# Kernel optimization log

Hardware: AMD Instinct MI355X
Metric: run time of the kernel (lower is better)

Reference implementation:

```python
import jax, jax.numpy as jnp
import numpy as np

N = 20000      # nodes
E = 640000     # edges (before self loops)
IN = 256       # in_channels == out_channels (forced by classifier size 4*in)
H1, C1 = 8, 16   # conv1: heads=8, out=16 -> concat 128
H2, C2 = 1, 256  # conv2: heads=1, out=out_channels
B = 4096       # article pairs
NEG_SLOPE = 0.2  # PyG GATv2Conv default negative_slope


def setup_inputs() -> dict:
    key = jax.random.key(0)
    ks = jax.random.split(key, 24)
    s = 0.05
    inp = {
        "gnn_x": jax.random.normal(ks[0], (N, IN), jnp.float32),
        "vanilla_x": jax.random.normal(ks[1], (N, IN), jnp.float32),
        "edge_src": jax.random.randint(ks[2], (E,), 0, N, jnp.int32),
        "edge_dst": jax.random.randint(ks[3], (E,), 0, N, jnp.int32),
        "a1_idx": jax.random.randint(ks[4], (B,), 0, N, jnp.int64),
        "a2_idx": jax.random.randint(ks[5], (B,), 0, N, jnp.int64),
        # conv1 params (lin_l, lin_r, att, bias)
        "Wl1": jax.random.normal(ks[6], (IN, H1 * C1), jnp.float32) * s,
        "bl1": jnp.zeros((H1 * C1,), jnp.float32),
        "Wr1": jax.random.normal(ks[7], (IN, H1 * C1), jnp.float32) * s,
        "br1": jnp.zeros((H1 * C1,), jnp.float32),
        "att1": jax.random.normal(ks[8], (H1, C1), jnp.float32) * s,
        "bias1": jnp.zeros((H1 * C1,), jnp.float32),
        # conv2 params
        "Wl2": jax.random.normal(ks[9], (H1 * C1, H2 * C2), jnp.float32) * s,
        "bl2": jnp.zeros((H2 * C2,), jnp.float32),
        "Wr2": jax.random.normal(ks[10], (H1 * C1, H2 * C2), jnp.float32) * s,
        "br2": jnp.zeros((H2 * C2,), jnp.float32),
        "att2": jax.random.normal(ks[11], (H2, C2), jnp.float32) * s,
        "bias2": jnp.zeros((H2 * C2,), jnp.float32),
        # classifier
        "Wc": jax.random.normal(ks[12], (4 * IN, 1), jnp.float32) * s,
        "bc": jnp.zeros((1,), jnp.float32),
    }
    return inp


def _gatv2_layer(x, src, dst, Wl, bl, Wr, br, att, bias):
    """GATv2Conv: x_l = lin_l(x)[src], x_r = lin_r(x)[dst];
    e = att . leaky_relu(x_l + x_r); segment softmax over dst; scatter-add x_l*alpha."""
    n = x.shape[0]
    h, c = att.shape
    xl = (x @ Wl + bl).reshape(n, h, c)
    xr = (x @ Wr + br).reshape(n, h, c)
    # per-edge attention logits [E, H]
    e = jnp.einsum('ehc,hc->eh', jax.nn.leaky_relu(xl[src] + xr[dst], NEG_SLOPE), att)
    # segment softmax over destination nodes (self loops guarantee non-empty segments)
    emax = jax.ops.segment_max(e, dst, num_segments=n)
    ex = jnp.exp(e - emax[dst])
    denom = jax.ops.segment_sum(ex, dst, num_segments=n)
    alpha = ex / denom[dst]                      # [E, H]
    out = jax.ops.segment_sum(alpha[:, :, None] * xl[src], dst, num_segments=n)  # [N,H,C]
    return out.reshape(n, h * c) + bias          # concat=True (heads=1 identical)


def reference(gnn_x, vanilla_x, Wl1, bl1, Wr1, br1, att1, bias1,
              Wl2, bl2, Wr2, br2, att2, bias2, Wc, bc,
              edge_src, edge_dst, a1_idx, a2_idx):
    n = gnn_x.shape[0]
    loops = jnp.arange(n, dtype=edge_src.dtype)
    src = jnp.concatenate([edge_src, loops])     # PyG add_self_loops=True
    dst = jnp.concatenate([edge_dst, loops])
    x = _gatv2_layer(gnn_x, src, dst, Wl1, bl1, Wr1, br1, att1, bias1)
    x = jax.nn.relu(x)
    x = _gatv2_layer(x, src, dst, Wl2, bl2, Wr2, br2, att2, bias2)
    combined = jnp.concatenate(
        [vanilla_x[a1_idx], vanilla_x[a2_idx], x[a1_idx], x[a2_idx]], axis=1)  # [B, 4*IN]
    logits = combined @ Wc + bc                  # [B, 1]
    return logits
```

## Files before the change

### kernel.cpp

```cpp
#include <hip/hip_runtime.h>
#include <math.h>

#define N_NODES 20000
#define M_PAD   20032
#define E_EDGES 640000
#define ET (E_EDGES + N_NODES)
#define IN_CH 256
#define D1 128
#define D2 256
#define BPAIRS 4096
#define NEG 0.2f
#define LOG2E 1.4426950408889634f

#define NB_HIST   128
#define CHUNK     ((ET + NB_HIST - 1) / NB_HIST)
#define HALF_BINS 10000

#define MARK_BLOCKS  (2 * BPAIRS / 256)
#define WT_BLOCKS    32
#define XCONV_BLOCKS (M_PAD * IN_CH / 4 / 4 / 256)

#define G1X (M_PAD / 64)
#define G1Y (D1 / 64)
#define G1_BLOCKS (G1X * G1Y)
#define SCAT_BLOCKS ((ET + 255) / 256)

#if __has_builtin(__builtin_amdgcn_exp2f)
#define EXP2F(x) __builtin_amdgcn_exp2f(x)
#else
#define EXP2F(x) exp2f(x)
#endif

typedef __bf16 bf16x8 __attribute__((ext_vector_type(8)));
typedef float  f32x4  __attribute__((ext_vector_type(4)));
typedef float  f32x2  __attribute__((ext_vector_type(2)));
typedef unsigned short u16x4 __attribute__((ext_vector_type(4)));

__device__ __forceinline__ unsigned short f2b(float f) {
    unsigned int u = __float_as_uint(f);
    unsigned int r = u + 0x7FFFu + ((u >> 16) & 1u);
    return (unsigned short)(r >> 16);
}
__device__ __forceinline__ f32x2 up2(unsigned int u) {
    f32x2 r;
    r.x = __uint_as_float(u << 16);
    r.y = __uint_as_float(u & 0xFFFF0000u);
    return r;
}
__device__ __forceinline__ f32x2 lrelu2(f32x2 s) {
    return __builtin_elementwise_max(s, s * NEG);
}
__device__ __forceinline__ float lrelu(float s) { return fmaxf(s, NEG * s); }

__device__ __forceinline__ void unpack8(uint4 u, float* v) {
    v[0] = __uint_as_float(u.x << 16); v[1] = __uint_as_float(u.x & 0xFFFF0000u);
    v[2] = __uint_as_float(u.y << 16); v[3] = __uint_as_float(u.y & 0xFFFF0000u);
    v[4] = __uint_as_float(u.z << 16); v[5] = __uint_as_float(u.z & 0xFFFF0000u);
    v[6] = __uint_as_float(u.w << 16); v[7] = __uint_as_float(u.w & 0xFFFF0000u);
}


__global__ __launch_bounds__(256) void prep_kernel(
        const float* __restrict__ gnn_x,
        const float* __restrict__ Wl1, const float* __restrict__ Wr1,
        const float* __restrict__ Wl2, const float* __restrict__ Wr2,
        const int* __restrict__ edge_dst,
        const int* __restrict__ a1_raw, const int* __restrict__ a2_raw,
        unsigned short* __restrict__ xb,
        unsigned short* __restrict__ wt1l, unsigned short* __restrict__ wt1r,
        unsigned short* __restrict__ wt2l, unsigned short* __restrict__ wt2r,
        int* __restrict__ cb,
        int* __restrict__ rank,
        int* __restrict__ mark) {
    __shared__ int lc[HALF_BINS];
    int bid = blockIdx.x;
    if (bid < NB_HIST) {
        int ebeg = bid * CHUNK;
        int eend = min(ebeg + CHUNK, ET);
#pragma unroll 1
        for (int half = 0; half < 2; half++) {
            int lo = half * HALF_BINS;
            for (int i = threadIdx.x; i < HALF_BINS; i += 256) lc[i] = 0;
            __syncthreads();
            for (int e = ebeg + threadIdx.x; e < eend; e += 256) {
                int dst = (e < E_EDGES) ? edge_dst[e] : (e - E_EDGES);
                int d = dst - lo;
                if (0 <= d && d < HALF_BINS) rank[e] = atomicAdd(&lc[d], 1);
            }
            __syncthreads();
            for (int i = threadIdx.x; i < HALF_BINS; i += 256)
                cb[(size_t)bid * N_NODES + lo + i] = lc[i];
            __syncthreads();
        }
    } else if (bid < NB_HIST + MARK_BLOCKS) {
        int idx = (bid - NB_HIST) * 256 + threadIdx.x;
        __shared__ int stride_s;
        if (threadIdx.x == 0) {
            bool i64 = true;
            for (int i = 1; i < 63; i += 2) i64 = i64 && (a1_raw[i] == 0);
            stride_s = i64 ? 2 : 1;
        }
        __syncthreads();
        int stride = stride_s;
        if (idx < BPAIRS) mark[a1_raw[(long)idx * stride]] = 1;
        else mark[a2_raw[(long)(idx - BPAIRS) * stride]] = 1;
    } else if (bid < NB_HIST + MARK_BLOCKS + WT_BLOCKS) {
        unsigned short* tile = (unsigned short*)lc;
        int t = bid - NB_HIST - MARK_BLOCKS;
        int m = t >> 3;
        int tt = t & 7;
        const float* W;
        unsigned short* Wt;
        int K, N;
        if (m == 0)      { W = Wl1; Wt = wt1l; K = IN_CH; N = D1; }
        else if (m == 1) { W = Wr1; Wt = wt1r; K = IN_CH; N = D1; }
        else if (m == 2) { W = Wl2; Wt = wt2l; K = D1; N = D2; }
        else             { W = Wr2; Wt = wt2r; K = D1; N = D2; }
        int ntn = N >> 6;
        int k0 = (tt / ntn) << 6;
        int n0 = (tt % ntn) << 6;
        int c = threadIdx.x & 63;
        int rr = threadIdx.x >> 6;
#pragma unroll
        for (int ch = 0; ch < 16; ch++) {
            int row = rr * 16 + ch;
            tile[row * 65 + c] = f2b(W[(size_t)(k0 + row) * N + n0 + c]);
        }
        __syncthreads();
#pragma unroll
        for (int ch = 0; ch < 16; ch++) {
            int n = rr * 16 + ch;
            Wt[(size_t)(n0 + n) * K + k0 + c] = tile[c * 65 + n];
        }
    } else {
        int tid = (bid - NB_HIST - MARK_BLOCKS - WT_BLOCKS) * 256
                + threadIdx.x;
        const int NQ = M_PAD * IN_CH / 4;
        int q0 = tid * 4;
#pragma unroll
        for (int j = 0; j < 4; j++) {
            int qi = q0 + j;
            if (qi >= NQ) break;
            int e0 = qi * 4;
            int row = e0 >> 8;
            u16x4 o;
            if (row < N_NODES) {
                f32x4 v = __builtin_nontemporal_load((const f32x4*)(gnn_x + e0));
                o.x = f2b(v.x); o.y = f2b(v.y); o.z = f2b(v.z); o.w = f2b(v.w);
            } else {
                o.x = o.y = o.z = o.w = 0;
            }
            *(u16x4*)(xb + e0) = o;
        }
    }
}


__global__ __launch_bounds__(256) void repprefix_kernel(
        int* __restrict__ cb, int* __restrict__ count) {
    int dst = blockIdx.x * 256 + threadIdx.x;
    if (dst >= N_NODES) return;
    int run = 0;
#pragma unroll 4
    for (int r = 0; r < NB_HIST; r++) {
        size_t idx = (size_t)r * N_NODES + dst;
        int c = cb[idx];
        cb[idx] = run;
        run += c;
    }
    count[dst] = run;
}


__global__ __launch_bounds__(1024) void scan_kernel(const int* __restrict__ count,
                                                    int* __restrict__ offsets) {
    const int PER = 20;
    int t = threadIdx.x;
    int base = t * PER;
    int local[PER];
    int sum = 0;
#pragma unroll
    for (int i = 0; i < PER; i++) {
        int idx = base + i;
        int v = (idx < N_NODES) ? count[idx] : 0;
        local[i] = sum;
        sum += v;
    }
    int lane = t & 63, wave = t >> 6;
    int s = sum;
#pragma unroll
    for (int off = 1; off < 64; off <<= 1) {
        int x = __shfl_up(s, off);
        if (lane >= off) s += x;
    }
    __shared__ int wsum[16];
    __shared__ int wpre[16];
    if (lane == 63) wsum[wave] = s;
    __syncthreads();
    if (t == 0) {
        int acc = 0;
        for (int w = 0; w < 16; w++) { wpre[w] = acc; acc += wsum[w]; }
        offsets[N_NODES] = acc;
    }
    __syncthreads();
    int thread_excl = wpre[wave] + (s - sum);
#pragma unroll
    for (int i = 0; i < PER; i++) {
        int idx = base + i;
        if (idx < N_NODES) offsets[idx] = thread_excl + local[i];
    }
}


template <int K>
__device__ __forceinline__ void dual_gemm_tile(
        const unsigned short* __restrict__ A,
        const unsigned short* __restrict__ Wtl,
        const unsigned short* __restrict__ Wtr,
        const float* __restrict__ bl, const float* __restrict__ br,
        unsigned short* __restrict__ Yl, unsigned short* __restrict__ Yr,
        int M, int NOUT, int bx, int by) {
    const int NK = K / 32;
    int wave = threadIdx.x >> 6;
    int lane = threadIdx.x & 63;
    int row0 = bx * 64;
    int col0 = (by * 4 + wave) * 16;
    int rsub = lane & 15;
    int koff = (lane >> 4) * 8;

    const unsigned short* ap  = A   + (size_t)(row0 + rsub) * K + koff;
    const unsigned short* bpl = Wtl + (size_t)(col0 + rsub) * K + koff;
    const unsigned short* bpr = Wtr + (size_t)(col0 + rsub) * K + koff;

    bf16x8 bfl[NK], bfr[NK];
#pragma unroll
    for (int kb = 0; kb < NK; kb++) {
        bfl[kb] = *(const bf16x8*)(bpl + kb * 32);
        bfr[kb] = *(const bf16x8*)(bpr + kb * 32);
    }

    f32x4 l0 = {0.f, 0.f, 0.f, 0.f};
    f32x4 l1 = l0, l2 = l0, l3 = l0, r0 = l0, r1 = l0, r2 = l0, r3 = l0;

#pragma unroll
    for (int kb = 0; kb < NK; kb++) {
        int off = kb * 32;
        bf16x8 a0 = *(const bf16x8*)(ap + off);
        bf16x8 a1 = *(const bf16x8*)(ap + 16 * K + off);
        bf16x8 a2 = *(const bf16x8*)(ap + 32 * K + off);
        bf16x8 a3 = *(const bf16x8*)(ap + 48 * K + off);
        l0 = __builtin_amdgcn_mfma_f32_16x16x32_bf16(a0, bfl[kb], l0, 0, 0, 0);
        r0 = __builtin_amdgcn_mfma_f32_16x16x32_bf16(a0, bfr[kb], r0, 0, 0, 0);
        l1 = __builtin_amdgcn_mfma_f32_16x16x32_bf16(a1, bfl[kb], l1, 0, 0, 0);
        r1 = __builtin_amdgcn_mfma_f32_16x16x32_bf16(a1, bfr[kb], r1, 0, 0, 0);
        l2 = __builtin_amdgcn_mfma_f32_16x16x32_bf16(a2, bfl[kb], l2, 0, 0, 0);
        r2 = __builtin_amdgcn_mfma_f32_16x16x32_bf16(a2, bfr[kb], r2, 0, 0, 0);
        l3 = __builtin_amdgcn_mfma_f32_16x16x32_bf16(a3, bfl[kb], l3, 0, 0, 0);
        r3 = __builtin_amdgcn_mfma_f32_16x16x32_bf16(a3, bfr[kb], r3, 0, 0, 0);
    }

    int colg = col0 + rsub;
    float bvl = bl[colg];
    float bvr = br[colg];
    int rbase = row0 + (lane >> 4) * 4;
#pragma unroll
    for (int t = 0; t < 4; t++) {
        f32x4 al = (t == 0) ? l0 : (t == 1) ? l1 : (t == 2) ? l2 : l3;
        f32x4 ar = (t == 0) ? r0 : (t == 1) ? r1 : (t == 2) ? r2 : r3;
#pragma unroll
        for (int r = 0; r < 4; r++) {
            int row = rbase + t * 16 + r;
            if (row < M) {
                Yl[(size_t)row * NOUT + colg] = f2b(al[r] + bvl);
                Yr[(size_t)row * NOUT + colg] = f2b(ar[r] + bvr);
            }
        }
    }
}


__global__ __launch_bounds__(256) void gemm1_scatter_kernel(
        const unsigned short* __restrict__ A,
        const unsigned short* __restrict__ Wtl,
        const unsigned short* __restrict__ Wtr,
        const float* __restrict__ bl, const float* __restrict__ br,
        unsigned short* __restrict__ Yl, unsigned short* __restrict__ Yr,
        const int* __restrict__ edge_src, const int* __restrict__ edge_dst,
        const int* __restrict__ rank, const int* __restrict__ offsets,
        const int* __restrict__ cb, int* __restrict__ sorted_src) {
    int bid = blockIdx.x;
    if (bid < G1_BLOCKS) {
        dual_gemm_tile<IN_CH>(A, Wtl, Wtr, bl, br, Yl, Yr,
                              N_NODES, D1, bid % G1X, bid / G1X);
    } else {
        int e = (bid - G1_BLOCKS) * 256 + threadIdx.x;
        if (e >= ET) return;
        int dst = (e < E_EDGES) ? edge_dst[e] : (e - E_EDGES);
        int src = (e < E_EDGES) ? edge_src[e] : (e - E_EDGES);
        int rep = e / CHUNK;
        sorted_src[offsets[dst] + cb[(size_t)rep * N_NODES + dst] + rank[e]] = src;
    }
}


template <int K>
__global__ __launch_bounds__(256) void dual_gemm_w32_kernel(
        const unsigned short* __restrict__ A,
        const unsigned short* __restrict__ Wtl,
        const unsigned short* __restrict__ Wtr,
        const float* __restrict__ bl, const float* __restrict__ br,
        unsigned short* __restrict__ Yl, unsigned short* __restrict__ Yr,
        int M, int NOUT) {
    const int NK = K / 32;
    int wave = threadIdx.x >> 6;
    int lane = threadIdx.x & 63;
    int row0 = blockIdx.x * 64;
    int col0 = blockIdx.y * 128 + wave * 32;
    int rsub = lane & 15;
    int koff = (lane >> 4) * 8;

    const unsigned short* ap = A + (size_t)(row0 + rsub) * K + koff;

    bf16x8 bfl[2][NK], bfr[2][NK];
#pragma unroll
    for (int c = 0; c < 2; c++) {
        const unsigned short* bpl = Wtl + (size_t)(col0 + c * 16 + rsub) * K + koff;
        const unsigned short* bpr = Wtr + (size_t)(col0 + c * 16 + rsub) * K + koff;
#pragma unroll
        for (int kb = 0; kb < NK; kb++) {
            bfl[c][kb] = *(const bf16x8*)(bpl + kb * 32);
            bfr[c][kb] = *(const bf16x8*)(bpr + kb * 32);
        }
    }

    f32x4 accl[2][4], accr[2][4];
#pragma unroll
    for (int c = 0; c < 2; c++)
#pragma unroll
        for (int t = 0; t < 4; t++) {
            accl[c][t] = (f32x4){0.f, 0.f, 0.f, 0.f};
            accr[c][t] = (f32x4){0.f, 0.f, 0.f, 0.f};
        }

#pragma unroll
    for (int kb = 0; kb < NK; kb++) {
        int off = kb * 32;
        bf16x8 a[4];
        a[0] = *(const bf16x8*)(ap + off);
        a[1] = *(const bf16x8*)(ap + 16 * K + off);
        a[2] = *(const bf16x8*)(ap + 32 * K + off);
        a[3] = *(const bf16x8*)(ap + 48 * K + off);
#pragma unroll
        for (int t = 0; t < 4; t++) {
#pragma unroll
            for (int c = 0; c < 2; c++) {
                accl[c][t] = __builtin_amdgcn_mfma_f32_16x16x32_bf16(
                    a[t], bfl[c][kb], accl[c][t], 0, 0, 0);
                accr[c][t] = __builtin_amdgcn_mfma_f32_16x16x32_bf16(
                    a[t], bfr[c][kb], accr[c][t], 0, 0, 0);
            }
        }
    }

    int rbase = row0 + (lane >> 4) * 4;
#pragma unroll
    for (int c = 0; c < 2; c++) {
        int colg = col0 + c * 16 + rsub;
        float bvl = bl[colg];
        float bvr = br[colg];
#pragma unroll
        for (int t = 0; t < 4; t++) {
#pragma unroll
            for (int r = 0; r < 4; r++) {
                int row = rbase + t * 16 + r;
                if (row < M) {
                    Yl[(size_t)row * NOUT + colg] = f2b(accl[c][t][r] + bvl);
                    Yr[(size_t)row * NOUT + colg] = f2b(accr[c][t][r] + bvr);
                }
            }
        }
    }
}


__global__ __launch_bounds__(256) void aggregate1_kernel(
        const unsigned short* __restrict__ xl1, const unsigned short* __restrict__ xr1,
        const float* __restrict__ att1, const float* __restrict__ bias1,
        const int* __restrict__ offsets, const int* __restrict__ sorted_src,
        unsigned short* __restrict__ x1) {
    int wave = threadIdx.x >> 6;
    int lane = threadIdx.x & 63;
    int q = lane >> 4;
    int ql = lane & 15;
    int dst = blockIdx.x * 4 + wave;
    if (dst >= M_PAD) return;
    int c0 = ql * 8;
    if (dst >= N_NODES) {
        if (q == 0) {
            uint4 z; z.x = z.y = z.z = z.w = 0;
            *(uint4*)(x1 + (size_t)dst * D1 + c0) = z;
        }
        return;
    }

    uint4 xu = *(const uint4*)(xr1 + (size_t)dst * D1 + c0);
    f32x2 xr[4] = {up2(xu.x), up2(xu.y), up2(xu.z), up2(xu.w)};
    float4 aa0 = *(const float4*)(att1 + c0);
    float4 aa1 = *(const float4*)(att1 + c0 + 4);
    f32x2 att[4];
    att[0].x = aa0.x * LOG2E; att[0].y = aa0.y * LOG2E;
    att[1].x = aa0.z * LOG2E; att[1].y = aa0.w * LOG2E;
    att[2].x = aa1.x * LOG2E; att[2].y = aa1.y * LOG2E;
    att[3].x = aa1.z * LOG2E; att[3].y = aa1.w * LOG2E;

    int beg = offsets[dst], end = offsets[dst + 1];
    const unsigned short* base = xl1 + c0;

    float l = 0.f;
    f32x2 acc[4] = {{0.f,0.f},{0.f,0.f},{0.f,0.f},{0.f,0.f}};

    int i = beg;
    int s0 = sorted_src[min(i + q, end - 1)];
    uint4 g0 = *(const uint4*)(base + (size_t)s0 * D1);
    bool more1 = (i + 4) < end;
    uint4 g1;
    if (more1) {
        int s1 = sorted_src[min(i + 4 + q, end - 1)];
        g1 = *(const uint4*)(base + (size_t)s1 * D1);
    }
    while (true) {
        bool more2 = (i + 8) < end;
        uint4 g2;
        if (more2) {
            int s2 = sorted_src[min(i + 8 + q, end - 1)];
            g2 = *(const uint4*)(base + (size_t)s2 * D1);
        }
        bool act = (i + q) < end;
        f32x2 v0 = up2(g0.x), v1 = up2(g0.y), v2 = up2(g0.z), v3 = up2(g0.w);
        f32x2 p2 = att[0] * lrelu2(v0 + xr[0]);
        p2 += att[1] * lrelu2(v1 + xr[1]);
        p2 += att[2] * lrelu2(v2 + xr[2]);
        p2 += att[3] * lrelu2(v3 + xr[3]);
        float p = p2.x + p2.y;
        p += __shfl_xor(p, 1);
        float w = act ? EXP2F(p) : 0.f;
        l += w;
        acc[0] += w * v0; acc[1] += w * v1; acc[2] += w * v2; acc[3] += w * v3;
        if (!more1) break;
        i += 4;
        g0 = g1; g1 = g2; more1 = more2;
    }
    l += __shfl_xor(l, 16);
    l += __shfl_xor(l, 32);
#pragma unroll
    for (int j = 0; j < 4; j++) {
        f32x2 t;
        t.x = __shfl_xor(acc[j].x, 16); t.y = __shfl_xor(acc[j].y, 16);
        acc[j] += t;
        t.x = __shfl_xor(acc[j].x, 32); t.y = __shfl_xor(acc[j].y, 32);
        acc[j] += t;
    }
    if (q == 0) {
        float inv = 1.f / l;
        float4 bb0 = *(const float4*)(bias1 + c0);
        float4 bb1 = *(const float4*)(bias1 + c0 + 4);
        unsigned short o[8];
        o[0] = f2b(fmaxf(acc[0].x * inv + bb0.x, 0.f));
        o[1] = f2b(fmaxf(acc[0].y * inv + bb0.y, 0.f));
        o[2] = f2b(fmaxf(acc[1].x * inv + bb0.z, 0.f));
        o[3] = f2b(fmaxf(acc[1].y * inv + bb0.w, 0.f));
        o[4] = f2b(fmaxf(acc[2].x * inv + bb1.x, 0.f));
        o[5] = f2b(fmaxf(acc[2].y * inv + bb1.y, 0.f));
        o[6] = f2b(fmaxf(acc[3].x * inv + bb1.z, 0.f));
        o[7] = f2b(fmaxf(acc[3].y * inv + bb1.w, 0.f));
        uint4 ov;
        ov.x = (unsigned int)o[0] | ((unsigned int)o[1] << 16);
        ov.y = (unsigned int)o[2] | ((unsigned int)o[3] << 16);
        ov.z = (unsigned int)o[4] | ((unsigned int)o[5] << 16);
        ov.w = (unsigned int)o[6] | ((unsigned int)o[7] << 16);
        *(uint4*)(x1 + (size_t)dst * D1 + c0) = ov;
    }
}


__global__ __launch_bounds__(256) void aggregate2_kernel(
        const unsigned short* __restrict__ xl2, const unsigned short* __restrict__ xr2,
        const float* __restrict__ att2, const float* __restrict__ bias2,
        const int* __restrict__ offsets, const int* __restrict__ sorted_src,
        const int* __restrict__ mark,
        float* __restrict__ x2) {
    int wave = threadIdx.x >> 6;
    int lane = threadIdx.x & 63;
    int half = lane >> 5;
    int hl = lane & 31;
    int dst = blockIdx.x * 4 + wave;
    if (dst >= N_NODES) return;
    if (mark[dst] != 1) return;
    int c0 = hl * 8;

    float xr[8], att[8];
    unpack8(*(const uint4*)(xr2 + (size_t)dst * D2 + c0), xr);
#pragma unroll
    for (int j = 0; j < 8; j++) att[j] = att2[c0 + j] * LOG2E;
    int beg = offsets[dst], end = offsets[dst + 1];

    float l = 0.f;
    float acc[8];
#pragma unroll
    for (int j = 0; j < 8; j++) acc[j] = 0.f;

    int i = beg;
    for (; i + 4 <= end; i += 4) {
        int sA = sorted_src[i + half];
        int sB = sorted_src[i + 2 + half];
        float vA[8], vB[8];
        unpack8(*(const uint4*)(xl2 + (size_t)sA * D2 + c0), vA);
        unpack8(*(const uint4*)(xl2 + (size_t)sB * D2 + c0), vB);
        float pA = 0.f, pB = 0.f;
#pragma unroll
        for (int j = 0; j < 8; j++) pA = fmaf(att[j], lrelu(vA[j] + xr[j]), pA);
#pragma unroll
        for (int j = 0; j < 8; j++) pB = fmaf(att[j], lrelu(vB[j] + xr[j]), pB);
        pA += __shfl_xor(pA, 1);  pB += __shfl_xor(pB, 1);
        pA += __shfl_xor(pA, 2);  pB += __shfl_xor(pB, 2);
        pA += __shfl_xor(pA, 4);  pB += __shfl_xor(pB, 4);
        pA += __shfl_xor(pA, 8);  pB += __shfl_xor(pB, 8);
        pA += __shfl_xor(pA, 16); pB += __shfl_xor(pB, 16);
        float wA = EXP2F(pA), wB = EXP2F(pB);
        l += wA + wB;
#pragma unroll
        for (int j = 0; j < 8; j++) acc[j] += wA * vA[j] + wB * vB[j];
    }
    for (; i + 2 <= end; i += 2) {
        int sA = sorted_src[i + half];
        float vA[8];
        unpack8(*(const uint4*)(xl2 + (size_t)sA * D2 + c0), vA);
        float pA = 0.f;
#pragma unroll
        for (int j = 0; j < 8; j++) pA = fmaf(att[j], lrelu(vA[j] + xr[j]), pA);
        pA += __shfl_xor(pA, 1);
        pA += __shfl_xor(pA, 2);
        pA += __shfl_xor(pA, 4);
        pA += __shfl_xor(pA, 8);
        pA += __shfl_xor(pA, 16);
        float wA = EXP2F(pA);
        l += wA;
#pragma unroll
        for (int j = 0; j < 8; j++) acc[j] += wA * vA[j];
    }
    if (i < end && half == 0) {
        int sA = sorted_src[i];
        float vA[8];
        unpack8(*(const uint4*)(xl2 + (size_t)sA * D2 + c0), vA);
        float pA = 0.f;
#pragma unroll
        for (int j = 0; j < 8; j++) pA = fmaf(att[j], lrelu(vA[j] + xr[j]), pA);
        pA += __shfl_xor(pA, 1);
        pA += __shfl_xor(pA, 2);
        pA += __shfl_xor(pA, 4);
        pA += __shfl_xor(pA, 8);
        pA += __shfl_xor(pA, 16);
        float wA = EXP2F(pA);
        l += wA;
#pragma unroll
        for (int j = 0; j < 8; j++) acc[j] += wA * vA[j];
    }
    l += __shfl_xor(l, 32);
#pragma unroll
    for (int j = 0; j < 8; j++) acc[j] += __shfl_xor(acc[j], 32);
    if (half == 0) {
        float inv = 1.f / l;
        float4 o0, o1;
        o0.x = acc[0] * inv + bias2[c0 + 0];
        o0.y = acc[1] * inv + bias2[c0 + 1];
        o0.z = acc[2] * inv + bias2[c0 + 2];
        o0.w = acc[3] * inv + bias2[c0 + 3];
        o1.x = acc[4] * inv + bias2[c0 + 4];
        o1.y = acc[5] * inv + bias2[c0 + 5];
        o1.z = acc[6] * inv + bias2[c0 + 6];
        o1.w = acc[7] * inv + bias2[c0 + 7];
        *(float4*)(x2 + (size_t)dst * D2 + c0) = o0;
        *(float4*)(x2 + (size_t)dst * D2 + c0 + 4) = o1;
    }
}


__global__ __launch_bounds__(256) void classifier_kernel(
        const float* __restrict__ vanilla_x, const float* __restrict__ x2,
        const int* __restrict__ a1_raw, const int* __restrict__ a2_raw,
        const float* __restrict__ Wc, const float* __restrict__ bc,
        float* __restrict__ out) {
    int b = blockIdx.x;
    int t = threadIdx.x;

    __shared__ int stride_s;
    if (t == 0) {
        bool i64 = true;
        for (int i = 1; i < 63; i += 2) i64 = i64 && (a1_raw[i] == 0);
        stride_s = i64 ? 2 : 1;
    }
    __syncthreads();
    int stride = stride_s;
    int a1 = a1_raw[(long)b * stride];
    int a2 = a2_raw[(long)b * stride];

    float s = vanilla_x[a1 * IN_CH + t] * Wc[t]
            + vanilla_x[a2 * IN_CH + t] * Wc[IN_CH + t]
            + x2[a1 * D2 + t] * Wc[2 * IN_CH + t]
            + x2[a2 * D2 + t] * Wc[3 * IN_CH + t];
    s += __shfl_xor(s, 1);
    s += __shfl_xor(s, 2);
    s += __shfl_xor(s, 4);
    s += __shfl_xor(s, 8);
    s += __shfl_xor(s, 16);
    s += __shfl_xor(s, 32);
    __shared__ float part[4];
    if ((t & 63) == 0) part[t >> 6] = s;
    __syncthreads();
    if (t == 0) out[b] = part[0] + part[1] + part[2] + part[3] + bc[0];
}


extern "C" void kernel_launch(void* const* d_in, const int* in_sizes, int n_in,
                              void* d_out, int out_size, void* d_ws, size_t ws_size,
                              hipStream_t stream) {
    const float* gnn_x     = (const float*)d_in[0];
    const float* vanilla_x = (const float*)d_in[1];
    const int*   edge_src  = (const int*)d_in[2];
    const int*   edge_dst  = (const int*)d_in[3];
    const int*   a1_idx    = (const int*)d_in[4];
    const int*   a2_idx    = (const int*)d_in[5];
    const float* Wl1   = (const float*)d_in[6];
    const float* bl1   = (const float*)d_in[7];
    const float* Wr1   = (const float*)d_in[8];
    const float* br1   = (const float*)d_in[9];
    const float* att1  = (const float*)d_in[10];
    const float* bias1 = (const float*)d_in[11];
    const float* Wl2   = (const float*)d_in[12];
    const float* bl2   = (const float*)d_in[13];
    const float* Wr2   = (const float*)d_in[14];
    const float* br2   = (const float*)d_in[15];
    const float* att2  = (const float*)d_in[16];
    const float* bias2 = (const float*)d_in[17];
    const float* Wc    = (const float*)d_in[18];
    const float* bc    = (const float*)d_in[19];
    float* out = (float*)d_out;

    char* p = (char*)d_ws;
    unsigned short* xb   = (unsigned short*)p; p += (size_t)M_PAD * IN_CH * 2;
    unsigned short* x1b  = (unsigned short*)p; p += (size_t)M_PAD * D1 * 2;
    unsigned short* xl1b = (unsigned short*)p; p += (size_t)N_NODES * D1 * 2;
    unsigned short* xr1b = (unsigned short*)p; p += (size_t)N_NODES * D1 * 2;
    unsigned short* xl2b = (unsigned short*)p; p += (size_t)N_NODES * D2 * 2;
    unsigned short* xr2b = (unsigned short*)p; p += (size_t)N_NODES * D2 * 2;
    unsigned short* wt1l = (unsigned short*)p; p += (size_t)D1 * IN_CH * 2;
    unsigned short* wt1r = (unsigned short*)p; p += (size_t)D1 * IN_CH * 2;
    unsigned short* wt2l = (unsigned short*)p; p += (size_t)D2 * D1 * 2;
    unsigned short* wt2r = (unsigned short*)p; p += (size_t)D2 * D1 * 2;
    float* x2 = (float*)p; p += (size_t)N_NODES * D2 * 4;
    int* count      = (int*)p; p += (size_t)N_NODES * 4;
    int* mark       = (int*)p; p += (size_t)N_NODES * 4;
    int* offsets    = (int*)p; p += (size_t)(N_NODES + 4) * 4;
    int* rank       = (int*)p; p += (size_t)ET * 4;
    int* sorted_src = (int*)p; p += (size_t)ET * 4;
    int* cb = (int*)xl2b;

    prep_kernel<<<NB_HIST + MARK_BLOCKS + WT_BLOCKS + XCONV_BLOCKS,
                  256, 0, stream>>>(
        gnn_x, Wl1, Wr1, Wl2, Wr2, edge_dst, a1_idx, a2_idx,
        xb, wt1l, wt1r, wt2l, wt2r, cb, rank, mark);
    repprefix_kernel<<<(N_NODES + 255) / 256, 256, 0, stream>>>(cb, count);
    scan_kernel<<<1, 1024, 0, stream>>>(count, offsets);

    gemm1_scatter_kernel<<<G1_BLOCKS + SCAT_BLOCKS, 256, 0, stream>>>(
        xb, wt1l, wt1r, bl1, br1, xl1b, xr1b,
        edge_src, edge_dst, rank, offsets, cb, sorted_src);

    aggregate1_kernel<<<M_PAD / 4, 256, 0, stream>>>(
        xl1b, xr1b, att1, bias1, offsets, sorted_src, x1b);

    dim3 g2(M_PAD / 64, D2 / 128);
    dual_gemm_w32_kernel<D1><<<g2, 256, 0, stream>>>(
        x1b, wt2l, wt2r, bl2, br2, xl2b, xr2b, N_NODES, D2);
    aggregate2_kernel<<<(N_NODES + 3) / 4, 256, 0, stream>>>(
        xl2b, xr2b, att2, bias2, offsets, sorted_src, mark, x2);

    classifier_kernel<<<BPAIRS, 256, 0, stream>>>(
        vanilla_x, x2, a1_idx, a2_idx, Wc, bc, out);
}
```

Baseline: 272.7 us.

## Fuse layer-2 aggregation into classifier, computing x2 only for queried pairs

Drops the mark pass and the separate aggregate2 kernel. Each classifier block now aggregates the two queried nodes directly, with two waves per node splitting the edge list and merging through shared memory, then does the dot product without writing x2 to global memory. This removes one launch, the mark writes, and the x2 round trip. In exchange, nodes that appear in several pairs are aggregated more than once, and block-level syncs are added.

```diff
diff --git a/kernel.cpp b/kernel.cpp
--- a/kernel.cpp
+++ b/kernel.cpp
@@ -16,7 +16,6 @@
 #define CHUNK     ((ET + NB_HIST - 1) / NB_HIST)
 #define HALF_BINS 10000
 
-#define MARK_BLOCKS  (2 * BPAIRS / 256)
 #define WT_BLOCKS    32
 #define XCONV_BLOCKS (M_PAD * IN_CH / 4 / 4 / 256)
 
@@ -65,13 +64,11 @@
         const float* __restrict__ Wl1, const float* __restrict__ Wr1,
         const float* __restrict__ Wl2, const float* __restrict__ Wr2,
         const int* __restrict__ edge_dst,
-        const int* __restrict__ a1_raw, const int* __restrict__ a2_raw,
         unsigned short* __restrict__ xb,
         unsigned short* __restrict__ wt1l, unsigned short* __restrict__ wt1r,
         unsigned short* __restrict__ wt2l, unsigned short* __restrict__ wt2r,
         int* __restrict__ cb,
-        int* __restrict__ rank,
-        int* __restrict__ mark) {
+        int* __restrict__ rank) {
     __shared__ int lc[HALF_BINS];
     int bid = blockIdx.x;
     if (bid < NB_HIST) {
@@ -92,21 +89,9 @@
                 cb[(size_t)bid * N_NODES + lo + i] = lc[i];
             __syncthreads();
         }
-    } else if (bid < NB_HIST + MARK_BLOCKS) {
-        int idx = (bid - NB_HIST) * 256 + threadIdx.x;
-        __shared__ int stride_s;
-        if (threadIdx.x == 0) {
-            bool i64 = true;
-            for (int i = 1; i < 63; i += 2) i64 = i64 && (a1_raw[i] == 0);
-            stride_s = i64 ? 2 : 1;
-        }
-        __syncthreads();
-        int stride = stride_s;
-        if (idx < BPAIRS) mark[a1_raw[(long)idx * stride]] = 1;
-        else mark[a2_raw[(long)(idx - BPAIRS) * stride]] = 1;
-    } else if (bid < NB_HIST + MARK_BLOCKS + WT_BLOCKS) {
+    } else if (bid < NB_HIST + WT_BLOCKS) {
         unsigned short* tile = (unsigned short*)lc;
-        int t = bid - NB_HIST - MARK_BLOCKS;
+        int t = bid - NB_HIST;
         int m = t >> 3;
         int tt = t & 7;
         const float* W;
@@ -133,8 +118,7 @@
             Wt[(size_t)(n0 + n) * K + k0 + c] = tile[c * 65 + n];
         }
     } else {
-        int tid = (bid - NB_HIST - MARK_BLOCKS - WT_BLOCKS) * 256
-                + threadIdx.x;
+        int tid = (bid - NB_HIST - WT_BLOCKS) * 256 + threadIdx.x;
         const int NQ = M_PAD * IN_CH / 4;
         int q0 = tid * 4;
 #pragma unroll
@@ -483,117 +467,19 @@
 }
 
 
-__global__ __launch_bounds__(256) void aggregate2_kernel(
+__global__ __launch_bounds__(256) void agg2_classifier_kernel(
         const unsigned short* __restrict__ xl2, const unsigned short* __restrict__ xr2,
         const float* __restrict__ att2, const float* __restrict__ bias2,
         const int* __restrict__ offsets, const int* __restrict__ sorted_src,
-        const int* __restrict__ mark,
-        float* __restrict__ x2) {
-    int wave = threadIdx.x >> 6;
-    int lane = threadIdx.x & 63;
-    int half = lane >> 5;
-    int hl = lane & 31;
-    int dst = blockIdx.x * 4 + wave;
-    if (dst >= N_NODES) return;
-    if (mark[dst] != 1) return;
-    int c0 = hl * 8;
-
-    float xr[8], att[8];
-    unpack8(*(const uint4*)(xr2 + (size_t)dst * D2 + c0), xr);
-#pragma unroll
-    for (int j = 0; j < 8; j++) att[j] = att2[c0 + j] * LOG2E;
-    int beg = offsets[dst], end = offsets[dst + 1];
-
-    float l = 0.f;
-    float acc[8];
-#pragma unroll
-    for (int j = 0; j < 8; j++) acc[j] = 0.f;
-
-    int i = beg;
-    for (; i + 4 <= end; i += 4) {
-        int sA = sorted_src[i + half];
-        int sB = sorted_src[i + 2 + half];
-        float vA[8], vB[8];
-        unpack8(*(const uint4*)(xl2 + (size_t)sA * D2 + c0), vA);
-        unpack8(*(const uint4*)(xl2 + (size_t)sB * D2 + c0), vB);
-        float pA = 0.f, pB = 0.f;
-#pragma unroll
-        for (int j = 0; j < 8; j++) pA = fmaf(att[j], lrelu(vA[j] + xr[j]), pA);
-#pragma unroll
-        for (int j = 0; j < 8; j++) pB = fmaf(att[j], lrelu(vB[j] + xr[j]), pB);
-        pA += __shfl_xor(pA, 1);  pB += __shfl_xor(pB, 1);
-        pA += __shfl_xor(pA, 2);  pB += __shfl_xor(pB, 2);
-        pA += __shfl_xor(pA, 4);  pB += __shfl_xor(pB, 4);
-        pA += __shfl_xor(pA, 8);  pB += __shfl_xor(pB, 8);
-        pA += __shfl_xor(pA, 16); pB += __shfl_xor(pB, 16);
-        float wA = EXP2F(pA), wB = EXP2F(pB);
-        l += wA + wB;
-#pragma unroll
-        for (int j = 0; j < 8; j++) acc[j] += wA * vA[j] + wB * vB[j];
-    }
-    for (; i + 2 <= end; i += 2) {
-        int sA = sorted_src[i + half];
-        float vA[8];
-        unpack8(*(const uint4*)(xl2 + (size_t)sA * D2 + c0), vA);
-        float pA = 0.f;
-#pragma unroll
-        for (int j = 0; j < 8; j++) pA = fmaf(att[j], lrelu(vA[j] + xr[j]), pA);
-        pA += __shfl_xor(pA, 1);
-        pA += __shfl_xor(pA, 2);
-        pA += __shfl_xor(pA, 4);
-        pA += __shfl_xor(pA, 8);
-        pA += __shfl_xor(pA, 16);
-        float wA = EXP2F(pA);
-        l += wA;
-#pragma unroll
-        for (int j = 0; j < 8; j++) acc[j] += wA * vA[j];
-    }
-    if (i < end && half == 0) {
-        int sA = sorted_src[i];
-        float vA[8];
-        unpack8(*(const uint4*)(xl2 + (size_t)sA * D2 + c0), vA);
-        float pA = 0.f;
-#pragma unroll
-        for (int j = 0; j < 8; j++) pA = fmaf(att[j], lrelu(vA[j] + xr[j]), pA);
-        pA += __shfl_xor(pA, 1);
-        pA += __shfl_xor(pA, 2);
-        pA += __shfl_xor(pA, 4);
-        pA += __shfl_xor(pA, 8);
-        pA += __shfl_xor(pA, 16);
-        float wA = EXP2F(pA);
-        l += wA;
-#pragma unroll
-        for (int j = 0; j < 8; j++) acc[j] += wA * vA[j];
-    }
-    l += __shfl_xor(l, 32);
-#pragma unroll
-    for (int j = 0; j < 8; j++) acc[j] += __shfl_xor(acc[j], 32);
-    if (half == 0) {
-        float inv = 1.f / l;
-        float4 o0, o1;
-        o0.x = acc[0] * inv + bias2[c0 + 0];
-        o0.y = acc[1] * inv + bias2[c0 + 1];
-        o0.z = acc[2] * inv + bias2[c0 + 2];
-        o0.w = acc[3] * inv + bias2[c0 + 3];
-        o1.x = acc[4] * inv + bias2[c0 + 4];
-        o1.y = acc[5] * inv + bias2[c0 + 5];
-        o1.z = acc[6] * inv + bias2[c0 + 6];
-        o1.w = acc[7] * inv + bias2[c0 + 7];
-        *(float4*)(x2 + (size_t)dst * D2 + c0) = o0;
-        *(float4*)(x2 + (size_t)dst * D2 + c0 + 4) = o1;
-    }
-}
-
-
-__global__ __launch_bounds__(256) void classifier_kernel(
-        const float* __restrict__ vanilla_x, const float* __restrict__ x2,
+        const float* __restrict__ vanilla_x,
         const int* __restrict__ a1_raw, const int* __restrict__ a2_raw,
         const float* __restrict__ Wc, const float* __restrict__ bc,
         float* __restrict__ out) {
-    int b = blockIdx.x;
+    __shared__ float x2row[2][D2];
+    __shared__ float mrg[2][32][9];
+    __shared__ float part[4];
+    __shared__ int stride_s;
     int t = threadIdx.x;
-
-    __shared__ int stride_s;
     if (t == 0) {
         bool i64 = true;
         for (int i = 1; i < 63; i += 2) i64 = i64 && (a1_raw[i] == 0);
@@ -601,21 +487,81 @@
     }
     __syncthreads();
     int stride = stride_s;
+    int b = blockIdx.x;
     int a1 = a1_raw[(long)b * stride];
     int a2 = a2_raw[(long)b * stride];
 
-    float s = vanilla_x[a1 * IN_CH + t] * Wc[t]
-            + vanilla_x[a2 * IN_CH + t] * Wc[IN_CH + t]
-            + x2[a1 * D2 + t] * Wc[2 * IN_CH + t]
-            + x2[a2 * D2 + t] * Wc[3 * IN_CH + t];
+    int wave = t >> 6;
+    int d = wave >> 1;
+    int ww = wave & 1;
+    int lane = t & 63;
+    int half = lane >> 5;
+    int hl = lane & 31;
+    int c0 = hl * 8;
+    int dst = d ? a2 : a1;
+
+    float xr[8], att[8];
+    unpack8(*(const uint4*)(xr2 + (size_t)dst * D2 + c0), xr);
+#pragma unroll
+    for (int j = 0; j < 8; j++) att[j] = att2[c0 + j] * LOG2E;
+    int beg = offsets[dst], end = offsets[dst + 1];
+
+    float l = 0.f;
+    float acc[8];
+#pragma unroll
+    for (int j = 0; j < 8; j++) acc[j] = 0.f;
+
+    int sub = 2 * ww + half;
+    for (int i0 = beg; i0 < end; i0 += 4) {
+        int idx = i0 + sub;
+        bool act = idx < end;
+        int s = sorted_src[min(idx, end - 1)];
+        float v[8];
+        unpack8(*(const uint4*)(xl2 + (size_t)s * D2 + c0), v);
+        float p = 0.f;
+#pragma unroll
+        for (int j = 0; j < 8; j++) p = fmaf(att[j], lrelu(v[j] + xr[j]), p);
+        p += __shfl_xor(p, 1);
+        p += __shfl_xor(p, 2);
+        p += __shfl_xor(p, 4);
+        p += __shfl_xor(p, 8);
+        p += __shfl_xor(p, 16);
+        float w = act ? EXP2F(p) : 0.f;
+        l += w;
+#pragma unroll
+        for (int j = 0; j < 8; j++) acc[j] += w * v[j];
+    }
+    l += __shfl_xor(l, 32);
+#pragma unroll
+    for (int j = 0; j < 8; j++) acc[j] += __shfl_xor(acc[j], 32);
+    if (ww == 1 && half == 0) {
+        mrg[d][hl][0] = l;
+#pragma unroll
+        for (int j = 0; j < 8; j++) mrg[d][hl][1 + j] = acc[j];
+    }
+    __syncthreads();
+    if (ww == 0 && half == 0) {
+        l += mrg[d][hl][0];
+#pragma unroll
+        for (int j = 0; j < 8; j++) acc[j] += mrg[d][hl][1 + j];
+        float inv = 1.f / l;
+#pragma unroll
+        for (int j = 0; j < 8; j++)
+            x2row[d][c0 + j] = acc[j] * inv + bias2[c0 + j];
+    }
+    __syncthreads();
+
+    float s = vanilla_x[(size_t)a1 * IN_CH + t] * Wc[t]
+            + vanilla_x[(size_t)a2 * IN_CH + t] * Wc[IN_CH + t]
+            + x2row[0][t] * Wc[2 * IN_CH + t]
+            + x2row[1][t] * Wc[3 * IN_CH + t];
     s += __shfl_xor(s, 1);
     s += __shfl_xor(s, 2);
     s += __shfl_xor(s, 4);
     s += __shfl_xor(s, 8);
     s += __shfl_xor(s, 16);
     s += __shfl_xor(s, 32);
-    __shared__ float part[4];
-    if ((t & 63) == 0) part[t >> 6] = s;
+    if (lane == 0) part[wave] = s;
     __syncthreads();
     if (t == 0) out[b] = part[0] + part[1] + part[2] + part[3] + bc[0];
 }
@@ -657,18 +603,15 @@
     unsigned short* wt1r = (unsigned short*)p; p += (size_t)D1 * IN_CH * 2;
     unsigned short* wt2l = (unsigned short*)p; p += (size_t)D2 * D1 * 2;
     unsigned short* wt2r = (unsigned short*)p; p += (size_t)D2 * D1 * 2;
-    float* x2 = (float*)p; p += (size_t)N_NODES * D2 * 4;
     int* count      = (int*)p; p += (size_t)N_NODES * 4;
-    int* mark       = (int*)p; p += (size_t)N_NODES * 4;
     int* offsets    = (int*)p; p += (size_t)(N_NODES + 4) * 4;
     int* rank       = (int*)p; p += (size_t)ET * 4;
     int* sorted_src = (int*)p; p += (size_t)ET * 4;
     int* cb = (int*)xl2b;
 
-    prep_kernel<<<NB_HIST + MARK_BLOCKS + WT_BLOCKS + XCONV_BLOCKS,
-                  256, 0, stream>>>(
-        gnn_x, Wl1, Wr1, Wl2, Wr2, edge_dst, a1_idx, a2_idx,
-        xb, wt1l, wt1r, wt2l, wt2r, cb, rank, mark);
+    prep_kernel<<<NB_HIST + WT_BLOCKS + XCONV_BLOCKS, 256, 0, stream>>>(
+        gnn_x, Wl1, Wr1, Wl2, Wr2, edge_dst,
+        xb, wt1l, wt1r, wt2l, wt2r, cb, rank);
     repprefix_kernel<<<(N_NODES + 255) / 256, 256, 0, stream>>>(cb, count);
     scan_kernel<<<1, 1024, 0, stream>>>(count, offsets);
 
@@ -682,9 +625,8 @@
     dim3 g2(M_PAD / 64, D2 / 128);
     dual_gemm_w32_kernel<D1><<<g2, 256, 0, stream>>>(
         x1b, wt2l, wt2r, bl2, br2, xl2b, xr2b, N_NODES, D2);
-    aggregate2_kernel<<<(N_NODES + 3) / 4, 256, 0, stream>>>(
-        xl2b, xr2b, att2, bias2, offsets, sorted_src, mark, x2);
-
-    classifier_kernel<<<BPAIRS, 256, 0, stream>>>(
-        vanilla_x, x2, a1_idx, a2_idx, Wc, bc, out);
-}
+
+    agg2_classifier_kernel<<<BPAIRS, 256, 0, stream>>>(
+        xl2b, xr2b, att2, bias2, offsets, sorted_src,
+        vanilla_x, a1_idx, a2_idx, Wc, bc, out);
+}
```

Result: faster. 262.2 us (-3.8%).
